# Performance work log

Measured on AMD Instinct MI355X. Metric: run time of the kernel, lower is better.

The kernel has to match this reference:

```python
import jax, jax.numpy as jnp
import numpy as np

BETA = 0.9
THRESH = 1.0
SLOPE = 50.0

@jax.custom_vjp
def spike(x):
    # heaviside with fast_sigmoid(slope=50) surrogate gradient
    return (x > 0).astype(x.dtype)

def _spike_fwd(x):
    return spike(x), x

def _spike_bwd(x, g):
    grad = g / (SLOPE * jnp.abs(x) + 1.0) ** 2
    return (grad,)

spike.defvjp(_spike_fwd, _spike_bwd)

def setup_inputs() -> dict:
    key = jax.random.key(0)
    ks = jax.random.split(key, 9)
    T, B, D, H, C = 100, 128, 2048, 2048, 100
    s_in, s_h = 1.0 / np.sqrt(D), 1.0 / np.sqrt(H)
    return {
        'x_seq': jax.random.normal(ks[0], (T, B, D), dtype=jnp.float32),
        'W1': jax.random.uniform(ks[1], (D, H), minval=-s_in, maxval=s_in, dtype=jnp.float32),
        'b1': jax.random.uniform(ks[2], (H,), minval=-s_in, maxval=s_in, dtype=jnp.float32),
        'W2': jax.random.uniform(ks[3], (H, H), minval=-s_h, maxval=s_h, dtype=jnp.float32),
        'b2': jax.random.uniform(ks[4], (H,), minval=-s_h, maxval=s_h, dtype=jnp.float32),
        'W3': jax.random.uniform(ks[5], (H, H), minval=-s_h, maxval=s_h, dtype=jnp.float32),
        'b3': jax.random.uniform(ks[6], (H,), minval=-s_h, maxval=s_h, dtype=jnp.float32),
        'Wo': jax.random.uniform(ks[7], (H, C), minval=-s_h, maxval=s_h, dtype=jnp.float32),
        'bo': jax.random.uniform(ks[8], (C,), minval=-s_h, maxval=s_h, dtype=jnp.float32),
    }

def _lif(cur, mem):
    # snntorch Leaky (reset-by-subtraction): reset uses previous membrane
    reset = (mem - THRESH > 0).astype(mem.dtype)
    mem_new = BETA * mem + cur - reset * THRESH
    spk = spike(mem_new - THRESH)
    return spk, mem_new

def reference(x_seq, W1, b1, W2, b2, W3, b3, Wo, bo):
    T, B, _ = x_seq.shape
    H = W1.shape[1]
    C = Wo.shape[1]
    mem0 = (jnp.zeros((B, H)), jnp.zeros((B, H)), jnp.zeros((B, H)), jnp.zeros((B, C)))
    spk_sum0 = jnp.zeros((B, C))

    def step(carry, x_t):
        (m1, m2, m3, mo), ssum = carry
        s1, m1 = _lif(x_t @ W1 + b1, m1)
        s2, m2 = _lif(s1 @ W2 + b2, m2)
        s3, m3 = _lif(s2 @ W3 + b3, m3)
        so, mo = _lif(s3 @ Wo + bo, mo)
        return ((m1, m2, m3, mo), ssum + so), None

    (_, spk_out_sum), _ = jax.lax.scan(step, (mem0, spk_sum0), x_seq)
    return spk_out_sum
```

## Files before the change

kernel.cpp:

```cpp
#include <hip/hip_runtime.h>

typedef short short8 __attribute__((ext_vector_type(8)));
typedef float f32x4 __attribute__((ext_vector_type(4)));
typedef int int4v __attribute__((ext_vector_type(4)));

#define TT 100
#define BB 128
#define HH 2048
#define CC 100
#define NBLK 256
#define CHUNK 20
#define NCH (TT / CHUNK)
#define NPHASE (NCH + 3)
#define SLOTW 8192

__device__ inline unsigned short f2bf(float f) {
  unsigned u = __float_as_uint(f);
  return (unsigned short)((u + 0x7FFF + ((u >> 16) & 1)) >> 16);
}
__device__ inline float bf2f(unsigned short b) {
  return __uint_as_float((unsigned)b << 16);
}

__global__ __launch_bounds__(256) void transpose_cvt(
    const float* __restrict__ W, unsigned short* __restrict__ Wt)
{
  __shared__ float t[32][33];
  int n0 = blockIdx.x * 32, k0 = blockIdx.y * 32;
  int tx = threadIdx.x, ty = threadIdx.y;
  #pragma unroll
  for (int j = 0; j < 4; ++j)
    t[ty + 8 * j][tx] = W[(size_t)(k0 + ty + 8 * j) * HH + n0 + tx];
  __syncthreads();
  #pragma unroll
  for (int j = 0; j < 4; ++j)
    Wt[(size_t)(n0 + ty + 8 * j) * HH + k0 + tx] = f2bf(t[tx][ty + 8 * j]);
}

__global__ __launch_bounds__(512) void cvt_x(
    const float* __restrict__ x, unsigned short* __restrict__ xb, long n8)
{
  long i = (long)blockIdx.x * blockDim.x + threadIdx.x;
  if (i >= n8) return;
  const float4* p = (const float4*)x + i * 2;
  float4 a = p[0], b = p[1];
  short8 pv;
  pv[0] = (short)f2bf(a.x); pv[1] = (short)f2bf(a.y);
  pv[2] = (short)f2bf(a.z); pv[3] = (short)f2bf(a.w);
  pv[4] = (short)f2bf(b.x); pv[5] = (short)f2bf(b.y);
  pv[6] = (short)f2bf(b.z); pv[7] = (short)f2bf(b.w);
  *(short8*)(xb + i * 8) = pv;
}

__global__ __launch_bounds__(256) void gemm_big_bf16(
    const unsigned short* __restrict__ Ab, const unsigned short* __restrict__ Wt,
    const float* __restrict__ bias, unsigned short* __restrict__ cur)
{
  __shared__ unsigned short As[128 * 128];
  __shared__ unsigned short Bs[64 * 128];
  const int tid = threadIdx.x;
  const int w = tid >> 6, l = tid & 63;
  const int wm = w & 1, wn = w >> 1;
  const int c16 = l & 15, g = l >> 4;
  const int n0 = blockIdx.x * 64, m0 = blockIdx.y * 128;
  f32x4 acc[4][2] = {};

  for (int k0 = 0; k0 < 2048; k0 += 128) {
    #pragma unroll
    for (int i = 0; i < 8; ++i) {
      int gg = tid + i * 256;
      int r = gg >> 4, gi = gg & 15;
      int kb = (gi * 16) ^ ((r & 7) << 4);
      const char* src = (const char*)(Ab + (size_t)(m0 + r) * HH + k0) + kb;
      *(int4v*)((char*)As + r * 256 + kb) = *(const int4v*)src;
    }
    #pragma unroll
    for (int i = 0; i < 4; ++i) {
      int gg = tid + i * 256;
      int r = gg >> 4, gi = gg & 15;
      int kb = (gi * 16) ^ ((r & 7) << 4);
      const char* bsrc = (const char*)(Wt + (size_t)(n0 + r) * HH + k0) + kb;
      *(int4v*)((char*)Bs + r * 256 + kb) = *(const int4v*)bsrc;
    }
    __syncthreads();
    #pragma unroll
    for (int kk = 0; kk < 4; ++kk) {
      int koff = (kk * 4 + g) * 16;
      short8 a[4], b[2];
      #pragma unroll
      for (int mi = 0; mi < 4; ++mi) {
        int mr = wm * 64 + mi * 16 + c16;
        a[mi] = *(short8*)((char*)As + mr * 256 + (koff ^ ((mr & 7) << 4)));
      }
      #pragma unroll
      for (int ni = 0; ni < 2; ++ni) {
        int nr = wn * 32 + ni * 16 + c16;
        b[ni] = *(short8*)((char*)Bs + nr * 256 + (koff ^ ((nr & 7) << 4)));
      }
      #pragma unroll
      for (int mi = 0; mi < 4; ++mi)
        #pragma unroll
        for (int ni = 0; ni < 2; ++ni)
          acc[mi][ni] = __builtin_amdgcn_mfma_f32_16x16x32_bf16(
              a[mi], b[ni], acc[mi][ni], 0, 0, 0);
    }
    __syncthreads();
  }
  #pragma unroll
  for (int mi = 0; mi < 4; ++mi)
    #pragma unroll
    for (int ni = 0; ni < 2; ++ni) {
      int col = n0 + wn * 32 + ni * 16 + c16;
      int rbase = m0 + wm * 64 + mi * 16 + g * 4;
      float bv = bias[col];
      #pragma unroll
      for (int j = 0; j < 4; ++j)
        cur[(size_t)(rbase + j) * HH + col] = f2bf(acc[mi][ni][j] + bv);
    }
}

__global__ __launch_bounds__(256) void gemm_big_f32(
    const float* __restrict__ A, const unsigned short* __restrict__ Wt,
    const float* __restrict__ bias, unsigned short* __restrict__ cur)
{
  __shared__ unsigned short As[128 * 128];
  __shared__ unsigned short Bs[64 * 128];
  const int tid = threadIdx.x;
  const int w = tid >> 6, l = tid & 63;
  const int wm = w & 1, wn = w >> 1;
  const int c16 = l & 15, g = l >> 4;
  const int n0 = blockIdx.x * 64, m0 = blockIdx.y * 128;
  f32x4 acc[4][2] = {};

  for (int k0 = 0; k0 < 2048; k0 += 128) {
    #pragma unroll
    for (int i = 0; i < 8; ++i) {
      int gg = tid + i * 256;
      int r = gg >> 4, gi = gg & 15;
      int kb = (gi * 16) ^ ((r & 7) << 4);
      const float* src = A + (size_t)(m0 + r) * HH + k0 + (kb >> 1);
      float4 f0 = *(const float4*)src, f1 = *(const float4*)(src + 4);
      short8 pv;
      pv[0] = (short)f2bf(f0.x); pv[1] = (short)f2bf(f0.y);
      pv[2] = (short)f2bf(f0.z); pv[3] = (short)f2bf(f0.w);
      pv[4] = (short)f2bf(f1.x); pv[5] = (short)f2bf(f1.y);
      pv[6] = (short)f2bf(f1.z); pv[7] = (short)f2bf(f1.w);
      *(int4v*)((char*)As + r * 256 + kb) = *(int4v*)&pv;
    }
    #pragma unroll
    for (int i = 0; i < 4; ++i) {
      int gg = tid + i * 256;
      int r = gg >> 4, gi = gg & 15;
      int kb = (gi * 16) ^ ((r & 7) << 4);
      const char* bsrc = (const char*)(Wt + (size_t)(n0 + r) * HH + k0) + kb;
      *(int4v*)((char*)Bs + r * 256 + kb) = *(const int4v*)bsrc;
    }
    __syncthreads();
    #pragma unroll
    for (int kk = 0; kk < 4; ++kk) {
      int koff = (kk * 4 + g) * 16;
      short8 a[4], b[2];
      #pragma unroll
      for (int mi = 0; mi < 4; ++mi) {
        int mr = wm * 64 + mi * 16 + c16;
        a[mi] = *(short8*)((char*)As + mr * 256 + (koff ^ ((mr & 7) << 4)));
      }
      #pragma unroll
      for (int ni = 0; ni < 2; ++ni) {
        int nr = wn * 32 + ni * 16 + c16;
        b[ni] = *(short8*)((char*)Bs + nr * 256 + (koff ^ ((nr & 7) << 4)));
      }
      #pragma unroll
      for (int mi = 0; mi < 4; ++mi)
        #pragma unroll
        for (int ni = 0; ni < 2; ++ni)
          acc[mi][ni] = __builtin_amdgcn_mfma_f32_16x16x32_bf16(
              a[mi], b[ni], acc[mi][ni], 0, 0, 0);
    }
    __syncthreads();
  }
  #pragma unroll
  for (int mi = 0; mi < 4; ++mi)
    #pragma unroll
    for (int ni = 0; ni < 2; ++ni) {
      int col = n0 + wn * 32 + ni * 16 + c16;
      int rbase = m0 + wm * 64 + mi * 16 + g * 4;
      float bv = bias[col];
      #pragma unroll
      for (int j = 0; j < 4; ++j)
        cur[(size_t)(rbase + j) * HH + col] = f2bf(acc[mi][ni][j] + bv);
    }
}

__global__ void init_kernel(unsigned* flags, int n)
{
  int i = blockIdx.x * blockDim.x + threadIdx.x;
  int stride = gridDim.x * blockDim.x;
  for (int j = i; j < n; j += stride) flags[j] = 0u;
}

#define MM(WORD, HF, SIDX, ACCV) { \
    unsigned h_ = (HF) ? ((unsigned)(WORD) >> 16) : ((unsigned)(WORD) & 0xFFFFu); \
    int4v af_; \
    af_[0] = (int)(((h_ & 15u) * 0x204081u) & 0x01010101u); \
    af_[1] = (int)((((h_ >> 4) & 15u) * 0x204081u) & 0x01010101u); \
    af_[2] = (int)((((h_ >> 8) & 15u) * 0x204081u) & 0x01010101u); \
    af_[3] = (int)(((h_ >> 12) * 0x204081u) & 0x01010101u); \
    int4v bq_ = *(const int4v*)(bpan + bbase + (((SIDX) * 64) ^ bswz)); \
    ACCV = __builtin_amdgcn_mfma_i32_16x16x64_i8(af_, bq_, ACCV, 0, 0, 0); }

#define STEP8(ACV, CH, ACCV) \
    MM(ACV[CH][0], 0, CH * 8 + 0, ACCV) MM(ACV[CH][0], 1, CH * 8 + 1, ACCV) \
    MM(ACV[CH][1], 0, CH * 8 + 2, ACCV) MM(ACV[CH][1], 1, CH * 8 + 3, ACCV) \
    MM(ACV[CH][2], 0, CH * 8 + 4, ACCV) MM(ACV[CH][2], 1, CH * 8 + 5, ACCV) \
    MM(ACV[CH][3], 0, CH * 8 + 6, ACCV) MM(ACV[CH][3], 1, CH * 8 + 7, ACCV)

#define LOADN(AN, TN) { \
    const char* sb_ = (const char*)(sinb + (size_t)(TN) * SLOTW); \
    AN[0] = *(const int4v*)(sb_ + abyte + 0 * 64); \
    AN[1] = *(const int4v*)(sb_ + abyte + 1 * 64); \
    AN[2] = *(const int4v*)(sb_ + abyte + 2 * 64); \
    AN[3] = *(const int4v*)(sb_ + abyte + 3 * 64); }

#define STEPB(AC, AN, T, DOPRE) { \
    if (DOPRE) LOADN(AN, (T) + 1); \
    int4v acc0_ = {0, 0, 0, 0}, acc1_ = {0, 0, 0, 0}; \
    STEP8(AC, 0, acc0_) STEP8(AC, 1, acc0_) \
    STEP8(AC, 2, acc1_) STEP8(AC, 3, acc1_) \
    int4v accs_ = acc0_ + acc1_; \
    unsigned long long bal0_, bal1_, bal2_, bal3_; \
    { float cv_ = (float)accs_[0] * scl + bv, mo_ = memb[0]; \
      float mn_ = 0.9f * mo_ + cv_ - ((mo_ > 1.f) ? 1.f : 0.f); \
      memb[0] = mn_; bal0_ = __ballot((int)(mn_ > 1.f)); } \
    { float cv_ = (float)accs_[1] * scl + bv, mo_ = memb[1]; \
      float mn_ = 0.9f * mo_ + cv_ - ((mo_ > 1.f) ? 1.f : 0.f); \
      memb[1] = mn_; bal1_ = __ballot((int)(mn_ > 1.f)); } \
    { float cv_ = (float)accs_[2] * scl + bv, mo_ = memb[2]; \
      float mn_ = 0.9f * mo_ + cv_ - ((mo_ > 1.f) ? 1.f : 0.f); \
      memb[2] = mn_; bal2_ = __ballot((int)(mn_ > 1.f)); } \
    { float cv_ = (float)accs_[3] * scl + bv, mo_ = memb[3]; \
      float mn_ = 0.9f * mo_ + cv_ - ((mo_ > 1.f) ? 1.f : 0.f); \
      memb[3] = mn_; bal3_ = __ballot((int)(mn_ > 1.f)); } \
    if (c16 == 0) { \
      unsigned short* so_ = (unsigned short*)(soutb + (size_t)(T) * SLOTW); \
      int rb_ = w * 16 + g * 4; \
      so_[(rb_ + 0) * 128 + ppos] = (unsigned short)((bal0_ >> (g * 16)) & 0xFFFFull); \
      so_[(rb_ + 1) * 128 + ppos] = (unsigned short)((bal1_ >> (g * 16)) & 0xFFFFull); \
      so_[(rb_ + 2) * 128 + ppos] = (unsigned short)((bal2_ >> (g * 16)) & 0xFFFFull); \
      so_[(rb_ + 3) * 128 + ppos] = (unsigned short)((bal3_ >> (g * 16)) & 0xFFFFull); \
    } }

__global__ __launch_bounds__(512, 1) void snn_persist(
    const unsigned short* __restrict__ cur1,
    const float* __restrict__ W2, const float* __restrict__ b2,
    const float* __restrict__ W3, const float* __restrict__ b3,
    const float* __restrict__ Wo, const float* __restrict__ bo,
    unsigned* __restrict__ s1b, unsigned* __restrict__ s2b,
    unsigned* __restrict__ s3b,
    float* __restrict__ outsum, unsigned* __restrict__ flags,
    unsigned* __restrict__ go)
{
  __shared__ char bpan[16 * 2048];
  __shared__ unsigned sow[CHUNK * 64];
  __shared__ unsigned long long swm[CHUNK];

  const int blk = blockIdx.x, tid = threadIdx.x;
  const int w = tid >> 6, l = tid & 63;
  const int c16 = l & 15, g = l >> 4;
  const bool isL2 = blk < 128;
  const int panel = blk & 127;
  const int n0c = panel * 16;
  const float* Wsrc = isL2 ? W2 : W3;
  const float* bias = isL2 ? b2 : b3;
  const int col = n0c + c16;

  float mx = 0.f;
  for (int s = 0; s < 32; ++s) {
    int kb = s * 64 + g * 16;
    #pragma unroll
    for (int e = 0; e < 16; ++e)
      mx = fmaxf(mx, fabsf(Wsrc[(size_t)(kb + e) * HH + col]));
  }
  mx = fmaxf(mx, __shfl_xor(mx, 16));
  mx = fmaxf(mx, __shfl_xor(mx, 32));
  const float scl = mx * (1.f / 127.f);
  const float rsc = (mx > 0.f) ? (127.f / mx) : 0.f;
  const float bv = bias[col];

  {
    int c = tid & 15, kg = tid >> 4;
    #pragma unroll
    for (int j = 0; j < 4; ++j) {
      int k16 = kg * 64 + j * 16;
      int4v q = {0, 0, 0, 0};
      #pragma unroll
      for (int e = 0; e < 16; ++e) {
        float v = Wsrc[(size_t)(k16 + e) * HH + col];
        int qi = (int)rintf(v * rsc);
        qi = qi > 127 ? 127 : (qi < -127 ? -127 : qi);
        q[e >> 2] |= (qi & 0xFF) << ((e & 3) * 8);
      }
      *(int4v*)(bpan + c * 2048 + (k16 ^ ((c & 7) << 4))) = q;
    }
  }
  __syncthreads();

  const int bbase = c16 * 2048 + g * 16;
  const int bswz = (c16 & 7) << 4;

  const int ppos = ((panel >> 5) << 5) + ((panel & 3) << 3) + ((panel >> 2) & 7);
  const int arow = w * 16 + c16;
  const int abyte = arow * 256 + g * 16;

  const int l1row = panel;
  const int l1colbase = (blk >> 7) * 1024;
  const int l1kap = (blk >> 7) * 64 + (tid >> 3);
  const int l1pos = (l1kap & ~31) + ((l1kap & 3) << 3) + ((l1kap >> 2) & 7);

  float m1a = 0.f, m1b = 0.f;
  f32x4 memb = {0.f, 0.f, 0.f, 0.f};
  float memo = 0.f, osumo = 0.f;
  const float boc = (!isL2 && tid < CC) ? bo[tid] : 0.f;

  for (int p = 0; p < NPHASE; ++p) {
    if (p < NCH) {
      #pragma unroll
      for (int half = 0; half < 2; ++half) {
        unsigned cw[10];
        #pragma unroll
        for (int st = 0; st < 10; ++st) {
          int t = p * CHUNK + half * 10 + st;
          cw[st] = *((const unsigned*)(cur1 +
                     ((size_t)t * BB + l1row) * HH + l1colbase) + tid);
        }
        #pragma unroll
        for (int st = 0; st < 10; ++st) {
          int t = p * CHUNK + half * 10 + st;
          float c0 = bf2f((unsigned short)(cw[st] & 0xFFFF));
          float c1 = bf2f((unsigned short)(cw[st] >> 16));
          float mn0 = 0.9f * m1a + c0 - ((m1a > 1.f) ? 1.f : 0.f);
          float mn1 = 0.9f * m1b + c1 - ((m1b > 1.f) ? 1.f : 0.f);
          m1a = mn0; m1b = mn1;
          unsigned v = (mn0 > 1.f ? 1u : 0u) | (mn1 > 1.f ? 2u : 0u);
          v |= ((unsigned)__shfl_xor((int)v, 1)) << 2;
          v |= ((unsigned)__shfl_xor((int)v, 2)) << 4;
          v |= ((unsigned)__shfl_xor((int)v, 4)) << 8;
          if ((tid & 7) == 0) {
            unsigned short* so = (unsigned short*)(s1b + (size_t)t * SLOTW)
                                 + l1row * 128;
            so[l1pos] = (unsigned short)v;
          }
        }
      }
    }

    int tch = p - (isL2 ? 1 : 2);
    if (tch >= 0 && tch < NCH) {
      const unsigned* sinb = isL2 ? s1b : s2b;
      unsigned* soutb = isL2 ? s2b : s3b;
      int4v A0[4], A1[4];
      LOADN(A0, tch * CHUNK);
      for (int st2 = 0; st2 < CHUNK; st2 += 2) {
        const int t0 = tch * CHUNK + st2;
        STEPB(A0, A1, t0, 1)
        STEPB(A1, A0, t0 + 1, st2 + 1 < CHUNK - 1)
      }
    }

    int oc = p - 3;
    if (!isL2 && oc >= 0 && oc < NCH) {
      int r = blk - 128;
      for (int i = tid; i < CHUNK * 64; i += 512)
        sow[i] = s3b[(size_t)(oc * CHUNK + (i >> 6)) * SLOTW + r * 64 + (i & 63)];
      __syncthreads();
      if (tid < CHUNK) {
        unsigned long long m = 0;
        for (int wd = 0; wd < 64; ++wd)
          if (sow[tid * 64 + wd]) m |= 1ull << wd;
        swm[tid] = m;
      }
      __syncthreads();
      if (tid < CC) {
        #pragma unroll 1
        for (int st = 0; st < CHUNK; ++st) {
          float curv = boc;
          unsigned long long m = swm[st];
          while (m) {
            int wd = (int)__ffsll((long long)m) - 1; m &= m - 1;
            unsigned wv2 = sow[st * 64 + wd];
            #pragma unroll
            for (int hf = 0; hf < 2; ++hf) {
              unsigned hv = hf ? (wv2 >> 16) : (wv2 & 0xFFFFu);
              int P = wd * 2 + hf;
              int kap = ((P >> 5) << 5) + ((P & 7) << 2) + ((P >> 3) & 3);
              while (hv) {
                int b = (int)__ffs(hv) - 1; hv &= hv - 1;
                curv += Wo[(size_t)(kap * 16 + b) * CC + tid];
              }
            }
          }
          float mo = memo;
          float mn = 0.9f * mo + curv - ((mo > 1.f) ? 1.f : 0.f);
          memo = mn;
          if (mn > 1.f) osumo += 1.f;
        }
      }
      __syncthreads();
    }

    if (p < NPHASE - 1) {
      unsigned gen = (unsigned)(p + 1);
      __syncthreads();
      if (tid == 0)
        __hip_atomic_store(&flags[blk * 32], gen, __ATOMIC_RELEASE,
                           __HIP_MEMORY_SCOPE_AGENT);
      if (blk == 0) {
        if (tid < NBLK) {
          int guard = 0;
          while (__hip_atomic_load(&flags[tid * 32], __ATOMIC_ACQUIRE,
                                   __HIP_MEMORY_SCOPE_AGENT) < gen) {
            __builtin_amdgcn_s_sleep(2);
            if (++guard > (1 << 22)) break;
          }
        }
        __syncthreads();
        if (tid == 0)
          __hip_atomic_store(go, gen, __ATOMIC_RELEASE,
                             __HIP_MEMORY_SCOPE_AGENT);
      } else {
        if (tid == 0) {
          int guard = 0;
          while (__hip_atomic_load(go, __ATOMIC_ACQUIRE,
                                   __HIP_MEMORY_SCOPE_AGENT) < gen) {
            __builtin_amdgcn_s_sleep(4);
            if (++guard > (1 << 22)) break;
          }
        }
        __syncthreads();
      }
    }
  }

  if (!isL2 && tid < CC)
    outsum[(blk - 128) * CC + tid] = osumo;
}

extern "C" void kernel_launch(void* const* d_in, const int* in_sizes, int n_in,
                              void* d_out, int out_size, void* d_ws, size_t ws_size,
                              hipStream_t stream)
{
  const float* x  = (const float*)d_in[0];
  const float* W1 = (const float*)d_in[1];
  const float* b1 = (const float*)d_in[2];
  const float* W2 = (const float*)d_in[3];
  const float* b2 = (const float*)d_in[4];
  const float* W3 = (const float*)d_in[5];
  const float* b3 = (const float*)d_in[6];
  const float* Wo = (const float*)d_in[7];
  const float* bo = (const float*)d_in[8];
  float* out = (float*)d_out;

  unsigned* flags = (unsigned*)d_ws;
  unsigned* go = flags + 8192;
  unsigned* s1b = flags + 16384;
  unsigned* s2b = s1b + (size_t)TT * SLOTW;
  unsigned* s3b = s2b + (size_t)TT * SLOTW;
  unsigned short* Wt1 = (unsigned short*)(s3b + (size_t)TT * SLOTW);
  unsigned short* cur1 = Wt1 + (size_t)HH * HH;
  unsigned short* xb = cur1 + (size_t)TT * BB * HH;
  size_t need_xb = (size_t)((char*)(xb + (size_t)TT * BB * HH) - (char*)d_ws);

  hipLaunchKernelGGL(init_kernel, dim3(32), dim3(256), 0, stream, flags, 16384);
  hipLaunchKernelGGL(transpose_cvt, dim3(64, 64), dim3(32, 8), 0, stream, W1, Wt1);
  if (ws_size >= need_xb) {
    long n8 = (long)TT * BB * HH / 8;
    hipLaunchKernelGGL(cvt_x, dim3((unsigned)((n8 + 511) / 512)), dim3(512),
                       0, stream, x, xb, n8);
    hipLaunchKernelGGL(gemm_big_bf16, dim3(HH / 64, (TT * BB) / 128), dim3(256),
                       0, stream, xb, Wt1, b1, cur1);
  } else {
    hipLaunchKernelGGL(gemm_big_f32, dim3(HH / 64, (TT * BB) / 128), dim3(256),
                       0, stream, x, Wt1, b1, cur1);
  }
  hipLaunchKernelGGL(snn_persist, dim3(NBLK), dim3(512), 0, stream,
                     cur1, W2, b2, W3, b3, Wo, bo,
                     s1b, s2b, s3b, out, flags, go);
}
```

Measured before the change: 712.7 us.

## Replace global phase barrier with per-stage dataflow flags between layers

Replaces the centralized grid-wide barrier (master block gathers all flags, then broadcasts a go signal) with per-stage producer flags. Layer-1 results are marked in f1, layer-2 panels wait only on f1 and mark f2, and layer-3 waits on f2 and marks f3, which the output stage waits on. This removes the serialization through block 0 and lets stages proceed as soon as their inputs are ready. It relies on a correct memory-fence and acquire/release protocol, and keeps the spin-guard timeouts.

```diff
diff --git a/kernel.cpp b/kernel.cpp
--- a/kernel.cpp
+++ b/kernel.cpp
@@ -197,6 +197,28 @@
   int i = blockIdx.x * blockDim.x + threadIdx.x;
   int stride = gridDim.x * blockDim.x;
   for (int j = i; j < n; j += stride) flags[j] = 0u;
+}
+
+__device__ inline void markflag(unsigned* f, int idx, unsigned val)
+{
+  __syncthreads();
+  if (threadIdx.x == 0) {
+    __threadfence();
+    __hip_atomic_store(&f[idx * 32], val, __ATOMIC_RELEASE,
+                       __HIP_MEMORY_SCOPE_AGENT);
+  }
+}
+__device__ inline void waitall(unsigned* f, int n, unsigned val)
+{
+  if (threadIdx.x < n) {
+    int guard = 0;
+    while (__hip_atomic_load(&f[threadIdx.x * 32], __ATOMIC_ACQUIRE,
+                             __HIP_MEMORY_SCOPE_AGENT) < val) {
+      __builtin_amdgcn_s_sleep(2);
+      if (++guard > (1 << 22)) break;
+    }
+  }
+  __syncthreads();
 }
 
 #define MM(WORD, HF, SIDX, ACCV) { \
@@ -257,8 +279,9 @@
     const float* __restrict__ Wo, const float* __restrict__ bo,
     unsigned* __restrict__ s1b, unsigned* __restrict__ s2b,
     unsigned* __restrict__ s3b,
-    float* __restrict__ outsum, unsigned* __restrict__ flags,
-    unsigned* __restrict__ go)
+    float* __restrict__ outsum,
+    unsigned* __restrict__ f1, unsigned* __restrict__ f2,
+    unsigned* __restrict__ f3)
 {
   __shared__ char bpan[16 * 2048];
   __shared__ unsigned sow[CHUNK * 64];
@@ -352,88 +375,76 @@
           }
         }
       }
-    }
-
-    int tch = p - (isL2 ? 1 : 2);
-    if (tch >= 0 && tch < NCH) {
-      const unsigned* sinb = isL2 ? s1b : s2b;
-      unsigned* soutb = isL2 ? s2b : s3b;
-      int4v A0[4], A1[4];
-      LOADN(A0, tch * CHUNK);
-      for (int st2 = 0; st2 < CHUNK; st2 += 2) {
-        const int t0 = tch * CHUNK + st2;
-        STEPB(A0, A1, t0, 1)
-        STEPB(A1, A0, t0 + 1, st2 + 1 < CHUNK - 1)
-      }
-    }
-
-    int oc = p - 3;
-    if (!isL2 && oc >= 0 && oc < NCH) {
-      int r = blk - 128;
-      for (int i = tid; i < CHUNK * 64; i += 512)
-        sow[i] = s3b[(size_t)(oc * CHUNK + (i >> 6)) * SLOTW + r * 64 + (i & 63)];
-      __syncthreads();
-      if (tid < CHUNK) {
-        unsigned long long m = 0;
-        for (int wd = 0; wd < 64; ++wd)
-          if (sow[tid * 64 + wd]) m |= 1ull << wd;
-        swm[tid] = m;
-      }
-      __syncthreads();
-      if (tid < CC) {
-        #pragma unroll 1
-        for (int st = 0; st < CHUNK; ++st) {
-          float curv = boc;
-          unsigned long long m = swm[st];
-          while (m) {
-            int wd = (int)__ffsll((long long)m) - 1; m &= m - 1;
-            unsigned wv2 = sow[st * 64 + wd];
-            #pragma unroll
-            for (int hf = 0; hf < 2; ++hf) {
-              unsigned hv = hf ? (wv2 >> 16) : (wv2 & 0xFFFFu);
-              int P = wd * 2 + hf;
-              int kap = ((P >> 5) << 5) + ((P & 7) << 2) + ((P >> 3) & 3);
-              while (hv) {
-                int b = (int)__ffs(hv) - 1; hv &= hv - 1;
-                curv += Wo[(size_t)(kap * 16 + b) * CC + tid];
+      markflag(f1, blk, (unsigned)(p + 1));
+    }
+
+    if (isL2) {
+      int tch = p - 1;
+      if (tch >= 0 && tch < NCH) {
+        waitall(f1, 256, (unsigned)(tch + 1));
+        const unsigned* sinb = s1b;
+        unsigned* soutb = s2b;
+        int4v A0[4], A1[4];
+        LOADN(A0, tch * CHUNK);
+        for (int st2 = 0; st2 < CHUNK; st2 += 2) {
+          const int t0 = tch * CHUNK + st2;
+          STEPB(A0, A1, t0, 1)
+          STEPB(A1, A0, t0 + 1, st2 + 1 < CHUNK - 1)
+        }
+        markflag(f2, panel, (unsigned)(tch + 1));
+      }
+    } else {
+      int tch = p - 2;
+      if (tch >= 0 && tch < NCH) {
+        waitall(f2, 128, (unsigned)(tch + 1));
+        const unsigned* sinb = s2b;
+        unsigned* soutb = s3b;
+        int4v A0[4], A1[4];
+        LOADN(A0, tch * CHUNK);
+        for (int st2 = 0; st2 < CHUNK; st2 += 2) {
+          const int t0 = tch * CHUNK + st2;
+          STEPB(A0, A1, t0, 1)
+          STEPB(A1, A0, t0 + 1, st2 + 1 < CHUNK - 1)
+        }
+        markflag(f3, panel, (unsigned)(tch + 1));
+      }
+      int oc = p - 3;
+      if (oc >= 0 && oc < NCH) {
+        waitall(f3, 128, (unsigned)(oc + 1));
+        int r = blk - 128;
+        for (int i = tid; i < CHUNK * 64; i += 512)
+          sow[i] = s3b[(size_t)(oc * CHUNK + (i >> 6)) * SLOTW + r * 64 + (i & 63)];
+        __syncthreads();
+        if (tid < CHUNK) {
+          unsigned long long m = 0;
+          for (int wd = 0; wd < 64; ++wd)
+            if (sow[tid * 64 + wd]) m |= 1ull << wd;
+          swm[tid] = m;
+        }
+        __syncthreads();
+        if (tid < CC) {
+          #pragma unroll 1
+          for (int st = 0; st < CHUNK; ++st) {
+            float curv = boc;
+            unsigned long long m = swm[st];
+            while (m) {
+              int wd = (int)__ffsll((long long)m) - 1; m &= m - 1;
+              unsigned wv2 = sow[st * 64 + wd];
+              #pragma unroll
+              for (int hf = 0; hf < 2; ++hf) {
+                unsigned hv = hf ? (wv2 >> 16) : (wv2 & 0xFFFFu);
+                int P = wd * 2 + hf;
+                int kap = ((P >> 5) << 5) + ((P & 7) << 2) + ((P >> 3) & 3);
+                while (hv) {
+                  int b = (int)__ffs(hv) - 1; hv &= hv - 1;
+                  curv += Wo[(size_t)(kap * 16 + b) * CC + tid];
+                }
               }
             }
-          }
-          float mo = memo;
-          float mn = 0.9f * mo + curv - ((mo > 1.f) ? 1.f : 0.f);
-          memo = mn;
-          if (mn > 1.f) osumo += 1.f;
-        }
-      }
-      __syncthreads();
-    }
-
-    if (p < NPHASE - 1) {
-      unsigned gen = (unsigned)(p + 1);
-      __syncthreads();
-      if (tid == 0)
-        __hip_atomic_store(&flags[blk * 32], gen, __ATOMIC_RELEASE,
-                           __HIP_MEMORY_SCOPE_AGENT);
-      if (blk == 0) {
-        if (tid < NBLK) {
-          int guard = 0;
-          while (__hip_atomic_load(&flags[tid * 32], __ATOMIC_ACQUIRE,
-                                   __HIP_MEMORY_SCOPE_AGENT) < gen) {
-            __builtin_amdgcn_s_sleep(2);
-            if (++guard > (1 << 22)) break;
-          }
-        }
-        __syncthreads();
-        if (tid == 0)
-          __hip_atomic_store(go, gen, __ATOMIC_RELEASE,
-                             __HIP_MEMORY_SCOPE_AGENT);
-      } else {
-        if (tid == 0) {
-          int guard = 0;
-          while (__hip_atomic_load(go, __ATOMIC_ACQUIRE,
-                                   __HIP_MEMORY_SCOPE_AGENT) < gen) {
-            __builtin_amdgcn_s_sleep(4);
-            if (++guard > (1 << 22)) break;
+            float mo = memo;
+            float mn = 0.9f * mo + curv - ((mo > 1.f) ? 1.f : 0.f);
+            memo = mn;
+            if (mn > 1.f) osumo += 1.f;
           }
         }
         __syncthreads();
@@ -461,7 +472,9 @@
   float* out = (float*)d_out;
 
   unsigned* flags = (unsigned*)d_ws;
-  unsigned* go = flags + 8192;
+  unsigned* f1 = flags;
+  unsigned* f2 = flags + 8192;
+  unsigned* f3 = flags + 12288;
   unsigned* s1b = flags + 16384;
   unsigned* s2b = s1b + (size_t)TT * SLOTW;
   unsigned* s3b = s2b + (size_t)TT * SLOTW;
@@ -484,5 +497,5 @@
   }
   hipLaunchKernelGGL(snn_persist, dim3(NBLK), dim3(512), 0, stream,
                      cur1, W2, b2, W3, b3, Wo, bo,
-                     s1b, s2b, s3b, out, flags, go);
-}
+                     s1b, s2b, s3b, out, f1, f2, f3);
+}
```

New measurement: 690.9 us. 3.1% less time.
